# Optimization experiments

Hardware: AMD Instinct MI355X
Metric: run time of the kernel (lower is better)

Reference implementation:

```python
import jax, jax.numpy as jnp
import numpy as np

NEURONS = 512
CHANNELS = 384
H, W = 13, 13
BATCH = 512


def setup_inputs() -> dict:
    key = jax.random.key(0)
    kx, ks, kd, kb = jax.random.split(key, 4)
    x = jax.random.normal(kx, (BATCH, CHANNELS, H, W), dtype=jnp.float32)
    W_s = jax.random.normal(ks, (NEURONS, H, W), dtype=jnp.float32)      # spatial readout per neuron
    W_d = jax.random.normal(kd, (NEURONS, CHANNELS), dtype=jnp.float32)  # channel readout (squeezed 1x1 conv kernel)
    W_b = jax.random.normal(kb, (1, NEURONS), dtype=jnp.float32)
    return {"x": x, "W_s": W_s, "W_d": W_d, "W_b": W_b}


def reference(x, W_s, W_d, W_b):
    # Original: out = einsum('bchw,nhw->bnchw') -> per-neuron 1x1 conv with W_d[n] -> sum over (c,h,w) -> + W_b
    # Mathematically: out[b,n] = sum_{c,h,w} x[b,c,h,w] * W_s[n,h,w] * W_d[n,c] + W_b[0,n]
    # Factorized into two contractions, avoiding the (b,n,c,h,w) intermediate.
    pooled = jnp.einsum('bchw,nhw->bnc', x, W_s)   # spatial weighted pooling: [B, N, C]
    out = jnp.einsum('bnc,nc->bn', pooled, W_d)    # channel readout: [B, N]
    return out + W_b
```

## Files before the change

kernel.cpp:

```cpp
#include <hip/hip_runtime.h>


#define B_   512
#define C_   384
#define N_   512
#define HW_  169
#define CT   128
#define SXR  200

#define WSF_ELEMS  ((size_t)32 * 6 * 64 * 8)
#define WDF_ELEMS  ((size_t)24 * 32 * 64 * 4)

typedef __bf16 bf16x8 __attribute__((ext_vector_type(8)));
typedef float f32x4  __attribute__((ext_vector_type(4)));
typedef float f32x4u __attribute__((ext_vector_type(4), aligned(4)));

__device__ __forceinline__ __bf16 f2bf(float f) {
  union { float f; unsigned u; } v; v.f = f;
  unsigned r = (v.u + 0x7FFFu + ((v.u >> 16) & 1u)) >> 16;
  unsigned short s = (unsigned short)r;
  return __builtin_bit_cast(__bf16, s);
}

__device__ __forceinline__ unsigned pack_trunc(float a, float b) {
  return __builtin_amdgcn_perm(__builtin_bit_cast(unsigned, b),
                               __builtin_bit_cast(unsigned, a), 0x07060302u);
}

__global__ __launch_bounds__(256)
void prep_aux_kernel(const float* __restrict__ Ws,
                     const float* __restrict__ Wd,
                     __bf16* __restrict__ wsf,
                     float* __restrict__ wdf) {
  int t = blockIdx.x * 256 + threadIdx.x;
  if (t < 12288) {
    int lane = t & 63;
    int fr   = t >> 6;
    int kb   = fr % 6;
    int nm   = fr / 6;
    int n    = nm * 16 + (lane & 15);
    int k0   = kb * 32 + (lane >> 4) * 8;
    const float* src = Ws + (size_t)n * HW_;
    bf16x8 v;
    #pragma unroll
    for (int j = 0; j < 8; ++j) {
      int k = k0 + j;
      float f = (k < HW_) ? src[k] : 0.f;
      v[j] = f2bf(f);
    }
    *(bf16x8*)(wsf + (size_t)t * 8) = v;
  } else {
    int t2 = t - 12288;
    int lane = t2 & 63;
    int fr   = t2 >> 6;
    int nm   = fr & 31;
    int cm   = fr >> 5;
    int n    = nm * 16 + (lane & 15);
    int c0   = cm * 16 + (lane >> 4) * 4;
    f32x4 w = *(const f32x4u*)(Wd + (size_t)n * C_ + c0);
    *(f32x4*)(wdf + (size_t)t2 * 4) = w;
  }
}

__global__ __launch_bounds__(256, 3)
void conv_fused(const float* __restrict__ x,
                const __bf16* __restrict__ wsf,
                const float* __restrict__ wdf,
                const float* __restrict__ Wb,
                float* __restrict__ out) {
  __shared__ __align__(16) __bf16 Xs[CT * SXR];
  __shared__ float red[4][64];

  const int tid  = threadIdx.x;
  const int id    = blockIdx.x;
  const int slot  = id & 7;
  const int t8    = id >> 3;
  const int c_blk = t8 % 3;
  const int b     = (t8 / 3) * 8 + slot;

  const int lane  = tid & 63;
  const int wv    = tid >> 6;
  const int cq    = (wv >> 1) * 64;
  const int nq    = (wv & 1) * 64;
  const int lrow  = lane & 15;
  const int lquad = lane >> 4;

  const float* src = x + ((size_t)b * C_ + (size_t)c_blk * CT) * HW_;
  #pragma unroll 4
  for (int p = 0; p < 24; ++p) {
    int i   = p * 256 + tid;
    int row = i / 48;
    int ch  = i - row * 48;
    const float* bp = src + row * HW_ + ch * 4;
    float v0 = 0.f, v1 = 0.f, v2 = 0.f, v3 = 0.f;
    if (ch < 42) {
      f32x4u t = *(const f32x4u*)bp;
      v0 = t[0]; v1 = t[1]; v2 = t[2]; v3 = t[3];
    } else if (ch == 42) {
      v0 = bp[0];
    }
    unsigned d0 = pack_trunc(v0, v1);
    unsigned d1 = pack_trunc(v2, v3);
    uint2 d; d.x = d0; d.y = d1;
    *(uint2*)&Xs[row * SXR + ch * 4] = d;
  }
  __syncthreads();

  const int cm0 = c_blk * 8 + (cq >> 4);

  #pragma unroll 1
  for (int nb = 0; nb < 4; ++nb) {
    const int nm0 = nb * 8 + (nq >> 4);
    const __bf16* bbase = wsf + ((size_t)nm0 * 6) * 512 + (size_t)lane * 8;

    const f32x4 zero = {0.f, 0.f, 0.f, 0.f};
    f32x4 acc[4][4];
    #pragma unroll
    for (int mi = 0; mi < 4; ++mi)
      #pragma unroll
      for (int ni = 0; ni < 4; ++ni)
        acc[mi][ni] = zero;

    #pragma unroll
    for (int kb = 0; kb < 6; ++kb) {
      bf16x8 afr[4], bfr[4];
      #pragma unroll
      for (int mi = 0; mi < 4; ++mi)
        afr[mi] = *(const bf16x8*)&Xs[(cq + mi * 16 + lrow) * SXR + kb * 32 + lquad * 8];
      #pragma unroll
      for (int ni = 0; ni < 4; ++ni)
        bfr[ni] = *(const bf16x8*)(bbase + ((size_t)ni * 6 + kb) * 512);
      #pragma unroll
      for (int mi = 0; mi < 4; ++mi)
        #pragma unroll
        for (int ni = 0; ni < 4; ++ni)
          acc[mi][ni] = __builtin_amdgcn_mfma_f32_16x16x32_bf16(
              afr[mi], bfr[ni], acc[mi][ni], 0, 0, 0);
    }

    float s[4] = {0.f, 0.f, 0.f, 0.f};
    #pragma unroll
    for (int ni = 0; ni < 4; ++ni) {
      #pragma unroll
      for (int mi = 0; mi < 4; ++mi) {
        const f32x4 w = *(const f32x4*)(wdf +
            (((size_t)(cm0 + mi) * 32 + (nm0 + ni)) * 64 + lane) * 4);
        s[ni] += acc[mi][ni][0] * w[0] + acc[mi][ni][1] * w[1]
               + acc[mi][ni][2] * w[2] + acc[mi][ni][3] * w[3];
      }
    }

    #pragma unroll
    for (int ni = 0; ni < 4; ++ni) {
      s[ni] += __shfl_xor(s[ni], 16, 64);
      s[ni] += __shfl_xor(s[ni], 32, 64);
    }
    if (lane < 16) {
      #pragma unroll
      for (int ni = 0; ni < 4; ++ni)
        red[wv][ni * 16 + lrow] = s[ni];
    }
    __syncthreads();

    if (tid < 128) {
      const int half = tid >> 6;
      const int idx  = tid & 63;
      const int n    = nb * 128 + tid;
      float v = red[half][idx] + red[half + 2][idx];
      if (c_blk == 0) v += Wb[n];
      atomicAdd(&out[(size_t)b * N_ + n], v);
    }
    __syncthreads();
  }
}


#define LDSS 104
#define KCH  96
#define NT   128

__global__ __launch_bounds__(256)
void conv_main_fallback(const float* __restrict__ x,
                        const float* __restrict__ Ws_g,
                        const float* __restrict__ Wd,
                        const float* __restrict__ Wb,
                        float* __restrict__ out) {
  __shared__ __align__(16) __bf16 Xs[CT][LDSS];
  __shared__ __align__(16) __bf16 Ws[NT][LDSS];

  const int tid   = threadIdx.x;
  const int n_blk = blockIdx.x;
  const int c_blk = blockIdx.y;
  const int b     = blockIdx.z;
  const int c0 = c_blk * CT;
  const int n0 = n_blk * NT;
  const int lane  = tid & 63;
  const int wv    = tid >> 6;
  const int cq    = (wv >> 1) * 64;
  const int nq    = (wv & 1) * 64;
  const int lrow  = lane & 15;
  const int lquad = lane >> 4;

  const f32x4 zero = {0.f, 0.f, 0.f, 0.f};
  f32x4 acc[4][4];
  #pragma unroll
  for (int mi = 0; mi < 4; ++mi)
    #pragma unroll
    for (int ni = 0; ni < 4; ++ni)
      acc[mi][ni] = zero;

  const float* xb  = x    + (size_t)b  * (C_ * HW_) + (size_t)c0 * HW_;
  const float* wsb = Ws_g + (size_t)n0 * HW_;

  for (int ch = 0; ch < 2; ++ch) {
    const int k0 = ch * KCH;
    __syncthreads();
    for (int e = tid; e < CT * KCH; e += 256) {
      int r   = e / KCH;
      int col = e - r * KCH;
      int k   = k0 + col;
      float vx = 0.f, vw = 0.f;
      if (k < HW_) {
        vx = xb [r * HW_ + k];
        vw = wsb[r * HW_ + k];
      }
      Xs[r][col] = f2bf(vx);
      Ws[r][col] = f2bf(vw);
    }
    __syncthreads();

    #pragma unroll
    for (int ks = 0; ks < 3; ++ks) {
      const int kc = ks * 32 + lquad * 8;
      bf16x8 afr[4], bfr[4];
      #pragma unroll
      for (int mi = 0; mi < 4; ++mi)
        afr[mi] = *(const bf16x8*)&Xs[cq + mi * 16 + lrow][kc];
      #pragma unroll
      for (int ni = 0; ni < 4; ++ni)
        bfr[ni] = *(const bf16x8*)&Ws[nq + ni * 16 + lrow][kc];
      #pragma unroll
      for (int mi = 0; mi < 4; ++mi)
        #pragma unroll
        for (int ni = 0; ni < 4; ++ni)
          acc[mi][ni] = __builtin_amdgcn_mfma_f32_16x16x32_bf16(
              afr[mi], bfr[ni], acc[mi][ni], 0, 0, 0);
    }
  }

  #pragma unroll
  for (int ni = 0; ni < 4; ++ni) {
    const int n = n0 + nq + ni * 16 + lrow;
    float sv = 0.f;
    #pragma unroll
    for (int mi = 0; mi < 4; ++mi) {
      const int cbase = c0 + cq + mi * 16 + lquad * 4;
      #pragma unroll
      for (int i = 0; i < 4; ++i)
        sv += acc[mi][ni][i] * Wd[(size_t)n * C_ + (cbase + i)];
    }
    sv += __shfl_xor(sv, 16, 64);
    sv += __shfl_xor(sv, 32, 64);
    if (lane < 16) {
      if (c_blk == 0 && cq == 0) sv += Wb[n];
      atomicAdd(&out[(size_t)b * N_ + n], sv);
    }
  }
}

extern "C" void kernel_launch(void* const* d_in, const int* in_sizes, int n_in,
                              void* d_out, int out_size, void* d_ws, size_t ws_size,
                              hipStream_t stream) {
  const float* x   = (const float*)d_in[0];
  const float* Wsp = (const float*)d_in[1];
  const float* Wd  = (const float*)d_in[2];
  const float* Wb  = (const float*)d_in[3];
  float* out = (float*)d_out;

  hipMemsetAsync(d_out, 0, (size_t)out_size * sizeof(float), stream);

  const size_t need = WSF_ELEMS * sizeof(__bf16) + WDF_ELEMS * sizeof(float);

  if (ws_size >= need) {
    __bf16* wsf = (__bf16*)d_ws;
    float*  wdf = (float*)(wsf + WSF_ELEMS);

    prep_aux_kernel<<<240, 256, 0, stream>>>(Wsp, Wd, wsf, wdf);
    conv_fused<<<1536, 256, 0, stream>>>(x, wsf, wdf, Wb, out);
  } else {
    dim3 grid(N_ / NT, C_ / CT, B_);
    conv_main_fallback<<<grid, 256, 0, stream>>>(x, Wsp, Wd, Wb, out);
  }
}
```

Measured before the change: 255.2 us.

## Shrink channel tile to 96, raise occupancy, batch reductions into one pass

The fused kernel now splits channels into four blocks of 96 instead of three of 128. This cuts the shared-memory tile and accumulator count so four blocks can reside per CU, and the grid grows to 2048 blocks. Per-nb partial sums are kept in registers and reduced once at the end, reusing the X tile's LDS as reduction scratch. This removes the per-iteration barriers and the separate reduction buffer. The cost is more global atomics per output row and more redundant W_s fragment loads across the extra channel blocks.

```diff
diff --git a/kernel.cpp b/kernel.cpp
--- a/kernel.cpp
+++ b/kernel.cpp
@@ -5,7 +5,7 @@
 #define C_   384
 #define N_   512
 #define HW_  169
-#define CT   128
+#define CT_F 96
 #define SXR  200
 
 #define WSF_ELEMS  ((size_t)32 * 6 * 64 * 8)
@@ -62,32 +62,31 @@
   }
 }
 
-__global__ __launch_bounds__(256, 3)
+__global__ __launch_bounds__(256, 4)
 void conv_fused(const float* __restrict__ x,
                 const __bf16* __restrict__ wsf,
                 const float* __restrict__ wdf,
                 const float* __restrict__ Wb,
                 float* __restrict__ out) {
-  __shared__ __align__(16) __bf16 Xs[CT * SXR];
-  __shared__ float red[4][64];
+  __shared__ __align__(16) __bf16 Xs[CT_F * SXR];
 
   const int tid  = threadIdx.x;
   const int id    = blockIdx.x;
   const int slot  = id & 7;
   const int t8    = id >> 3;
-  const int c_blk = t8 % 3;
-  const int b     = (t8 / 3) * 8 + slot;
+  const int c_blk = t8 & 3;
+  const int b     = (t8 >> 2) * 8 + slot;
 
   const int lane  = tid & 63;
   const int wv    = tid >> 6;
-  const int cq    = (wv >> 1) * 64;
-  const int nq    = (wv & 1) * 64;
+  const int cq    = (wv >> 1) * 48;
+  const int nq4   = (wv & 1) * 4;
   const int lrow  = lane & 15;
   const int lquad = lane >> 4;
 
-  const float* src = x + ((size_t)b * C_ + (size_t)c_blk * CT) * HW_;
-  #pragma unroll 4
-  for (int p = 0; p < 24; ++p) {
+  const float* src = x + ((size_t)b * C_ + (size_t)c_blk * CT_F) * HW_;
+  #pragma unroll 6
+  for (int p = 0; p < 18; ++p) {
     int i   = p * 256 + tid;
     int row = i / 48;
     int ch  = i - row * 48;
@@ -106,75 +105,93 @@
   }
   __syncthreads();
 
-  const int cm0 = c_blk * 8 + (cq >> 4);
-
-  #pragma unroll 1
+  const int cm0 = c_blk * 6 + (cq >> 4);
+
+  float s[4][4];
+  #pragma unroll
+  for (int nb = 0; nb < 4; ++nb)
+    #pragma unroll
+    for (int ni = 0; ni < 4; ++ni)
+      s[nb][ni] = 0.f;
+
+  #pragma unroll
   for (int nb = 0; nb < 4; ++nb) {
-    const int nm0 = nb * 8 + (nq >> 4);
+    const int nm0 = nb * 8 + nq4;
     const __bf16* bbase = wsf + ((size_t)nm0 * 6) * 512 + (size_t)lane * 8;
 
     const f32x4 zero = {0.f, 0.f, 0.f, 0.f};
-    f32x4 acc[4][4];
-    #pragma unroll
-    for (int mi = 0; mi < 4; ++mi)
+    f32x4 acc[3][4];
+    #pragma unroll
+    for (int mi = 0; mi < 3; ++mi)
       #pragma unroll
       for (int ni = 0; ni < 4; ++ni)
         acc[mi][ni] = zero;
 
     #pragma unroll
     for (int kb = 0; kb < 6; ++kb) {
-      bf16x8 afr[4], bfr[4];
-      #pragma unroll
-      for (int mi = 0; mi < 4; ++mi)
+      bf16x8 afr[3], bfr[4];
+      #pragma unroll
+      for (int mi = 0; mi < 3; ++mi)
         afr[mi] = *(const bf16x8*)&Xs[(cq + mi * 16 + lrow) * SXR + kb * 32 + lquad * 8];
       #pragma unroll
       for (int ni = 0; ni < 4; ++ni)
         bfr[ni] = *(const bf16x8*)(bbase + ((size_t)ni * 6 + kb) * 512);
       #pragma unroll
-      for (int mi = 0; mi < 4; ++mi)
+      for (int mi = 0; mi < 3; ++mi)
         #pragma unroll
         for (int ni = 0; ni < 4; ++ni)
           acc[mi][ni] = __builtin_amdgcn_mfma_f32_16x16x32_bf16(
               afr[mi], bfr[ni], acc[mi][ni], 0, 0, 0);
     }
 
-    float s[4] = {0.f, 0.f, 0.f, 0.f};
+    const float* wbase = wdf + ((size_t)cm0 * 32 + nm0) * 256 + (size_t)lane * 4;
     #pragma unroll
     for (int ni = 0; ni < 4; ++ni) {
-      #pragma unroll
-      for (int mi = 0; mi < 4; ++mi) {
-        const f32x4 w = *(const f32x4*)(wdf +
-            (((size_t)(cm0 + mi) * 32 + (nm0 + ni)) * 64 + lane) * 4);
-        s[ni] += acc[mi][ni][0] * w[0] + acc[mi][ni][1] * w[1]
-               + acc[mi][ni][2] * w[2] + acc[mi][ni][3] * w[3];
+      float t = 0.f;
+      #pragma unroll
+      for (int mi = 0; mi < 3; ++mi) {
+        const f32x4 w = *(const f32x4*)(wbase + ((size_t)mi * 32 + ni) * 256);
+        t += acc[mi][ni][0] * w[0] + acc[mi][ni][1] * w[1]
+           + acc[mi][ni][2] * w[2] + acc[mi][ni][3] * w[3];
       }
-    }
-
+      s[nb][ni] = t;
+    }
+  }
+
+  #pragma unroll
+  for (int nb = 0; nb < 4; ++nb)
     #pragma unroll
     for (int ni = 0; ni < 4; ++ni) {
-      s[ni] += __shfl_xor(s[ni], 16, 64);
-      s[ni] += __shfl_xor(s[ni], 32, 64);
-    }
-    if (lane < 16) {
+      s[nb][ni] += __shfl_xor(s[nb][ni], 16, 64);
+      s[nb][ni] += __shfl_xor(s[nb][ni], 32, 64);
+    }
+
+  __syncthreads();
+  float* red = reinterpret_cast<float*>(Xs);
+  if (lane < 16) {
+    #pragma unroll
+    for (int nb = 0; nb < 4; ++nb)
       #pragma unroll
       for (int ni = 0; ni < 4; ++ni)
-        red[wv][ni * 16 + lrow] = s[ni];
-    }
-    __syncthreads();
-
-    if (tid < 128) {
-      const int half = tid >> 6;
-      const int idx  = tid & 63;
-      const int n    = nb * 128 + tid;
-      float v = red[half][idx] + red[half + 2][idx];
-      if (c_blk == 0) v += Wb[n];
-      atomicAdd(&out[(size_t)b * N_ + n], v);
-    }
-    __syncthreads();
-  }
-}
-
-
+        red[wv * 256 + nb * 64 + ni * 16 + lrow] = s[nb][ni];
+  }
+  __syncthreads();
+
+  #pragma unroll
+  for (int r = 0; r < 2; ++r) {
+    const int n   = r * 256 + tid;
+    const int nb  = n >> 7;
+    const int rem = n & 127;
+    const int h   = rem >> 6;
+    const int idx = rem & 63;
+    float v = red[h * 256 + nb * 64 + idx] + red[(h + 2) * 256 + nb * 64 + idx];
+    if (c_blk == 0) v += Wb[n];
+    atomicAdd(&out[(size_t)b * N_ + n], v);
+  }
+}
+
+
+#define CT   128
 #define LDSS 104
 #define KCH  96
 #define NT   128
@@ -286,7 +303,7 @@
     float*  wdf = (float*)(wsf + WSF_ELEMS);
 
     prep_aux_kernel<<<240, 256, 0, stream>>>(Wsp, Wd, wsf, wdf);
-    conv_fused<<<1536, 256, 0, stream>>>(x, wsf, wdf, Wb, out);
+    conv_fused<<<2048, 256, 0, stream>>>(x, wsf, wdf, Wb, out);
   } else {
     dim3 grid(N_ / NT, C_ / CT, B_);
     conv_main_fallback<<<grid, 256, 0, stream>>>(x, Wsp, Wd, Wb, out);
```

Result: slower. 299.1 us (+17.2%).

## Split channels into four partial slabs and reduce partials without atomics

Applied to the files above, without the earlier changes.

Adds a path that splits each batch's channels into four 96-channel blocks (2048 blocks, 4 per CU target). Each wave covers all 96 channels for two neuron tiles, so the cross-wave LDS reduction and per-nb syncthreads go away. Partial sums are written to a workspace buffer, and a separate kernel adds the four partials plus bias. This removes the output memset and the global atomics. The cost is an extra kernel launch and a 4MB partial buffer round-trip, and the path only runs when the workspace is large enough.

```diff
diff --git a/kernel.cpp b/kernel.cpp
--- a/kernel.cpp
+++ b/kernel.cpp
@@ -5,11 +5,13 @@
 #define C_   384
 #define N_   512
 #define HW_  169
+#define CT_F 96
 #define CT   128
 #define SXR  200
 
 #define WSF_ELEMS  ((size_t)32 * 6 * 64 * 8)
 #define WDF_ELEMS  ((size_t)24 * 32 * 64 * 4)
+#define PART_ELEMS ((size_t)4 * B_ * N_)
 
 typedef __bf16 bf16x8 __attribute__((ext_vector_type(8)));
 typedef float f32x4  __attribute__((ext_vector_type(4)));
@@ -62,12 +64,120 @@
   }
 }
 
+__global__ __launch_bounds__(256, 4)
+void conv_part(const float* __restrict__ x,
+               const __bf16* __restrict__ wsf,
+               const float* __restrict__ wdf,
+               float* __restrict__ part) {
+  __shared__ __align__(16) __bf16 Xs[CT_F * SXR];
+
+  const int tid  = threadIdx.x;
+  const int id    = blockIdx.x;
+  const int slot  = id & 7;
+  const int t8    = id >> 3;
+  const int c_blk = t8 & 3;
+  const int b     = (t8 >> 2) * 8 + slot;
+
+  const int lane  = tid & 63;
+  const int wv    = tid >> 6;
+  const int lrow  = lane & 15;
+  const int lquad = lane >> 4;
+
+  const float* src = x + ((size_t)b * C_ + (size_t)c_blk * CT_F) * HW_;
+  #pragma unroll 6
+  for (int p = 0; p < 18; ++p) {
+    int i   = p * 256 + tid;
+    int row = i / 48;
+    int ch  = i - row * 48;
+    const float* bp = src + row * HW_ + ch * 4;
+    float v0 = 0.f, v1 = 0.f, v2 = 0.f, v3 = 0.f;
+    if (ch < 42) {
+      f32x4u t = *(const f32x4u*)bp;
+      v0 = t[0]; v1 = t[1]; v2 = t[2]; v3 = t[3];
+    } else if (ch == 42) {
+      v0 = bp[0];
+    }
+    unsigned d0 = pack_trunc(v0, v1);
+    unsigned d1 = pack_trunc(v2, v3);
+    uint2 d; d.x = d0; d.y = d1;
+    *(uint2*)&Xs[row * SXR + ch * 4] = d;
+  }
+  __syncthreads();
+
+  float* pb = part + ((size_t)c_blk * B_ + b) * N_;
+
+  #pragma unroll 1
+  for (int nb = 0; nb < 4; ++nb) {
+    const int nm0 = nb * 8 + wv * 2;
+    const __bf16* bbase = wsf + ((size_t)nm0 * 6) * 512 + (size_t)lane * 8;
+
+    const f32x4 zero = {0.f, 0.f, 0.f, 0.f};
+    f32x4 acc[6][2];
+    #pragma unroll
+    for (int mi = 0; mi < 6; ++mi)
+      #pragma unroll
+      for (int ni = 0; ni < 2; ++ni)
+        acc[mi][ni] = zero;
+
+    #pragma unroll
+    for (int kb = 0; kb < 6; ++kb) {
+      bf16x8 afr[6], bfr[2];
+      #pragma unroll
+      for (int mi = 0; mi < 6; ++mi)
+        afr[mi] = *(const bf16x8*)&Xs[(mi * 16 + lrow) * SXR + kb * 32 + lquad * 8];
+      #pragma unroll
+      for (int ni = 0; ni < 2; ++ni)
+        bfr[ni] = *(const bf16x8*)(bbase + ((size_t)ni * 6 + kb) * 512);
+      #pragma unroll
+      for (int mi = 0; mi < 6; ++mi)
+        #pragma unroll
+        for (int ni = 0; ni < 2; ++ni)
+          acc[mi][ni] = __builtin_amdgcn_mfma_f32_16x16x32_bf16(
+              afr[mi], bfr[ni], acc[mi][ni], 0, 0, 0);
+    }
+
+    #pragma unroll
+    for (int ni = 0; ni < 2; ++ni) {
+      float t = 0.f;
+      #pragma unroll
+      for (int mi = 0; mi < 6; ++mi) {
+        const f32x4 w = *(const f32x4*)(wdf +
+            (((size_t)(c_blk * 6 + mi) * 32 + (nm0 + ni)) * 256 + (size_t)lane * 4));
+        t += acc[mi][ni][0] * w[0] + acc[mi][ni][1] * w[1]
+           + acc[mi][ni][2] * w[2] + acc[mi][ni][3] * w[3];
+      }
+      t += __shfl_xor(t, 16, 64);
+      t += __shfl_xor(t, 32, 64);
+      if (lane < 16)
+        pb[(nm0 + ni) * 16 + lrow] = t;
+    }
+  }
+}
+
+__global__ __launch_bounds__(256)
+void reduce_part(const float* __restrict__ part,
+                 const float* __restrict__ Wb,
+                 float* __restrict__ out) {
+  const size_t S = (size_t)B_ * N_;
+  int idx = (blockIdx.x * 256 + threadIdx.x) * 4;
+  f32x4 a0 = *(const f32x4u*)(part + idx);
+  f32x4 a1 = *(const f32x4u*)(part + S + idx);
+  f32x4 a2 = *(const f32x4u*)(part + 2 * S + idx);
+  f32x4 a3 = *(const f32x4u*)(part + 3 * S + idx);
+  f32x4 wb = *(const f32x4u*)(Wb + (idx & (N_ - 1)));
+  f32x4 r;
+  #pragma unroll
+  for (int i = 0; i < 4; ++i)
+    r[i] = a0[i] + a1[i] + a2[i] + a3[i] + wb[i];
+  *(f32x4*)(out + idx) = r;
+}
+
 __global__ __launch_bounds__(256, 3)
-void conv_fused(const float* __restrict__ x,
-                const __bf16* __restrict__ wsf,
-                const float* __restrict__ wdf,
-                const float* __restrict__ Wb,
-                float* __restrict__ out) {
+void conv_fused_v8(const float* __restrict__ x,
+                   const __bf16* __restrict__ wsf,
+                   const float* __restrict__ wdf,
+                   const float* __restrict__ Wb,
+                   float* __restrict__ out) {
   __shared__ __align__(16) __bf16 Xs[CT * SXR];
   __shared__ float red[4][64];
 
@@ -277,17 +387,26 @@
   const float* Wb  = (const float*)d_in[3];
   float* out = (float*)d_out;
 
-  hipMemsetAsync(d_out, 0, (size_t)out_size * sizeof(float), stream);
-
-  const size_t need = WSF_ELEMS * sizeof(__bf16) + WDF_ELEMS * sizeof(float);
-
-  if (ws_size >= need) {
+  const size_t need_basic = WSF_ELEMS * sizeof(__bf16) + WDF_ELEMS * sizeof(float);
+  const size_t need_full  = need_basic + PART_ELEMS * sizeof(float);
+
+  if (ws_size >= need_full) {
+    __bf16* wsf  = (__bf16*)d_ws;
+    float*  wdf  = (float*)(wsf + WSF_ELEMS);
+    float*  partb = wdf + WDF_ELEMS;
+
+    prep_aux_kernel<<<240, 256, 0, stream>>>(Wsp, Wd, wsf, wdf);
+    conv_part<<<2048, 256, 0, stream>>>(x, wsf, wdf, partb);
+    reduce_part<<<256, 256, 0, stream>>>(partb, Wb, out);
+  } else if (ws_size >= need_basic) {
     __bf16* wsf = (__bf16*)d_ws;
     float*  wdf = (float*)(wsf + WSF_ELEMS);
 
+    hipMemsetAsync(d_out, 0, (size_t)out_size * sizeof(float), stream);
     prep_aux_kernel<<<240, 256, 0, stream>>>(Wsp, Wd, wsf, wdf);
-    conv_fused<<<1536, 256, 0, stream>>>(x, wsf, wdf, Wb, out);
+    conv_fused_v8<<<1536, 256, 0, stream>>>(x, wsf, wdf, Wb, out);
   } else {
+    hipMemsetAsync(d_out, 0, (size_t)out_size * sizeof(float), stream);
     dim3 grid(N_ / NT, C_ / CT, B_);
     conv_main_fallback<<<grid, 256, 0, stream>>>(x, Wsp, Wd, Wb, out);
   }
```

Result: slower. 412.2 us (+61.5%).
